# Kernel optimization log

Measured on AMD Instinct MI355X. Metric: run time of the kernel, lower is better.

Reference implementation:

```python
import jax, jax.numpy as jnp
import numpy as np
import math

K_HEADS = 16  # nb_heads from init_kwargs


def setup_inputs() -> dict:
    key = jax.random.key(0)
    ks = jax.random.split(key, 7)
    B, M, H, D = 2, 2048, 1024, 1024 // K_HEADS
    return {
        "h": jax.random.normal(ks[0], (B, M, H), jnp.float32),
        "h_cache": jax.random.normal(ks[1], (B, M, H), jnp.float32),
        "key_pe": jax.random.normal(ks[2], (1, D, M), jnp.float32),
        "Wq": jax.random.normal(ks[3], (H, H), jnp.float32) * 0.02,
        "Wk": jax.random.normal(ks[4], (H, H), jnp.float32) * 0.02,
        "Wv": jax.random.normal(ks[5], (H, H), jnp.float32) * 0.02,
        "Wo": jax.random.normal(ks[6], (H, H), jnp.float32) * 0.02,
    }


def _heads(x, K):
    # [B, M, H] -> [B, K, M, D]
    B, M, H = x.shape
    return x.reshape(B, M, K, H // K).transpose(0, 2, 1, 3)


def reference(h, h_cache, key_pe, Wq, Wk, Wv, Wo):
    B, M, H = h.shape
    K = K_HEADS
    D = H // K
    q = _heads(h @ Wq.T, K)        # [B, K, M, D]
    k = _heads(h_cache @ Wk.T, K)  # [B, K, L, D], L == M
    v = _heads(h_cache @ Wv.T, K)  # [B, K, L, D]

    attn_cont = jnp.einsum("bkmd,bkld->bkml", q, k)            # content scores
    attn_pos = jnp.einsum("bkmd,dl->bkml", q, key_pe[0])       # positional scores
    attn = (attn_cont + attn_pos[..., :M]) / math.sqrt(D)
    attn = jax.nn.softmax(attn, axis=-1)  # computed as in source, but source
    # (faithfully) multiplies VALUE by attn_cont, not attn:
    out = jnp.einsum("bkml,bkld->bkmd", attn_cont, v)          # [B, K, M, D]
    out = out.transpose(0, 2, 1, 3).reshape(B, M, H)
    return out @ Wo.T
```

## Files before the change

kernel.cpp:

```cpp
#include <hip/hip_runtime.h>
#include <hip/hip_bf16.h>

#define BB 2
#define MM 2048
#define HH 1024
#define KH 16

typedef short s16x8 __attribute__((ext_vector_type(8)));
typedef float f32x4 __attribute__((ext_vector_type(4)));
typedef float f32x16 __attribute__((ext_vector_type(16)));

#define GLOBAL_AS __attribute__((address_space(1)))
#define LDS_AS    __attribute__((address_space(3)))

__device__ __forceinline__ void async_copy16(const void* g, void* l) {
    __builtin_amdgcn_global_load_lds((const GLOBAL_AS void*)g, (LDS_AS void*)l, 16, 0, 0);
}

struct __align__(8) bf16x4_t { __hip_bfloat16 x, y, z, w; };

__global__ __launch_bounds__(256) void cvt_all(
    const float* __restrict__ s0, const float* __restrict__ s1,
    const float* __restrict__ s2, const float* __restrict__ s3,
    const float* __restrict__ s4, const float* __restrict__ Wq,
    __hip_bfloat16* __restrict__ d0, __hip_bfloat16* __restrict__ d1,
    __hip_bfloat16* __restrict__ d2, __hip_bfloat16* __restrict__ d3,
    __hip_bfloat16* __restrict__ d4, __hip_bfloat16* __restrict__ WqT,
    float* __restrict__ Sz)
{
    const int seg = blockIdx.y;
    const int t = threadIdx.x;
    if (seg == 5) {
        const int bx = blockIdx.x;
        if (bx < 128) {
            const int i = (bx * 256 + t) * 4;
            float4 z = {0.f, 0.f, 0.f, 0.f};
            *(float4*)(Sz + i) = z;
        } else if (bx < 384) {
            __shared__ float Tl[64][65];
            const int tile = bx - 128;
            const int j0 = (tile >> 4) * 64;
            const int k0 = (tile & 15) * 64;
            const int r = t >> 6;
            const int c = t & 63;
#pragma unroll
            for (int i = 0; i < 64; i += 4)
                Tl[r + i][c] = Wq[(size_t)(j0 + r + i) * HH + k0 + c];
            __syncthreads();
#pragma unroll
            for (int i = 0; i < 64; i += 4)
                WqT[(size_t)(k0 + r + i) * HH + j0 + c] = __float2bfloat16(Tl[c][r + i]);
        }
        return;
    }
    const float* src;
    __hip_bfloat16* dst;
    int n;
    switch (seg) {
        case 0: src = s0; dst = d0; n = BB * MM * HH; break;
        case 1: src = s1; dst = d1; n = BB * MM * HH; break;
        case 2: src = s2; dst = d2; n = HH * HH; break;
        case 3: src = s3; dst = d3; n = HH * HH; break;
        default: src = s4; dst = d4; n = HH * HH; break;
    }
    const int i = (blockIdx.x * 256 + t) * 4;
    if (i + 3 < n) {
        const float4 v = *(const float4*)(src + i);
        bf16x4_t o;
        o.x = __float2bfloat16(v.x);
        o.y = __float2bfloat16(v.y);
        o.z = __float2bfloat16(v.z);
        o.w = __float2bfloat16(v.w);
        *(bf16x4_t*)(dst + i) = o;
    }
}

__device__ __forceinline__ void store_c(__hip_bfloat16* C, size_t idx, float v) {
    C[idx] = __float2bfloat16(v);
}
__device__ __forceinline__ void store_c(float* C, size_t idx, float v) { C[idx] = v; }

#define LP2 136

__global__ __launch_bounds__(256) void gemm_kvt(
    const __hip_bfloat16* __restrict__ hcb,
    const __hip_bfloat16* __restrict__ wk, const __hip_bfloat16* __restrict__ wv,
    float* __restrict__ S)
{
    __shared__ __align__(16) char smem[64 * LP2 * 2 * 2];
    __hip_bfloat16* As  = (__hip_bfloat16*)smem;
    __hip_bfloat16* Bsk = (__hip_bfloat16*)(smem + 16384);
    __hip_bfloat16* Bsv = (__hip_bfloat16*)(smem + 24576);
    __hip_bfloat16* Kt  = (__hip_bfloat16*)smem;
    __hip_bfloat16* Vt  = (__hip_bfloat16*)(smem + 64 * LP2 * 2);

    const int t    = threadIdx.x;
    const int lane = t & 63;
    const int wave = t >> 6;
    const int head = blockIdx.y;
    const int m0   = blockIdx.x * 128;
    const int n0   = head * 64;
    const int b    = blockIdx.x >> 4;

    const int srow = lane >> 3;
    const int sw   = ((lane & 7) ^ srow) * 8;

    const int wm  = (wave >> 1) * 64;
    const int wn  = (wave & 1) * 32;
    const int fm  = lane & 31;
    const int fm7 = fm & 7;
    const int ghi = lane >> 5;

    f32x16 acck[2] = {};
    f32x16 accv[2] = {};

    for (int k0 = 0; k0 < HH; k0 += 64) {
        __syncthreads();
#pragma unroll
        for (int i = 0; i < 4; ++i) {
            const int c = wave * 4 + i;
            async_copy16(hcb + (size_t)(m0 + c * 8 + srow) * HH + k0 + sw,
                         As + c * 512);
        }
#pragma unroll
        for (int i = 0; i < 2; ++i) {
            const int c = wave * 2 + i;
            async_copy16(wk + (size_t)(n0 + c * 8 + srow) * HH + k0 + sw,
                         Bsk + c * 512);
            async_copy16(wv + (size_t)(n0 + c * 8 + srow) * HH + k0 + sw,
                         Bsv + c * 512);
        }
        __syncthreads();

#pragma unroll
        for (int ks = 0; ks < 64; ks += 16) {
            const int pos = ((((ks >> 3) + ghi) ^ fm7) * 8);
            s16x8 af[2];
#pragma unroll
            for (int mi = 0; mi < 2; ++mi)
                af[mi] = *(const s16x8*)(As + (wm + mi * 32 + fm) * 64 + pos);
            const s16x8 bk = *(const s16x8*)(Bsk + (wn + fm) * 64 + pos);
            const s16x8 bv = *(const s16x8*)(Bsv + (wn + fm) * 64 + pos);
#pragma unroll
            for (int mi = 0; mi < 2; ++mi) {
                acck[mi] = __builtin_amdgcn_mfma_f32_32x32x16_bf16(af[mi], bk, acck[mi], 0, 0, 0);
                accv[mi] = __builtin_amdgcn_mfma_f32_32x32x16_bf16(af[mi], bv, accv[mi], 0, 0, 0);
            }
        }
    }

    __syncthreads();

    const int dcol = wn + (lane & 31);
    const int lhi  = 4 * (lane >> 5);
#pragma unroll
    for (int mi = 0; mi < 2; ++mi)
#pragma unroll
        for (int g = 0; g < 4; ++g) {
            const int lb = wm + mi * 32 + 8 * g + lhi;
            bf16x4_t ok, ov;
            ok.x = __float2bfloat16(acck[mi][4 * g + 0]);
            ok.y = __float2bfloat16(acck[mi][4 * g + 1]);
            ok.z = __float2bfloat16(acck[mi][4 * g + 2]);
            ok.w = __float2bfloat16(acck[mi][4 * g + 3]);
            ov.x = __float2bfloat16(accv[mi][4 * g + 0]);
            ov.y = __float2bfloat16(accv[mi][4 * g + 1]);
            ov.z = __float2bfloat16(accv[mi][4 * g + 2]);
            ov.w = __float2bfloat16(accv[mi][4 * g + 3]);
            *(bf16x4_t*)(Kt + dcol * LP2 + lb) = ok;
            *(bf16x4_t*)(Vt + dcol * LP2 + lb) = ov;
        }
    __syncthreads();

    const int fr = lane & 15;
    const int fq = (lane >> 4) * 8;
    const int wm2 = wave * 16;

    f32x4 acc2[4] = {};
#pragma unroll
    for (int kk = 0; kk < 128; kk += 32) {
        const s16x8 af = *(const s16x8*)(Kt + (wm2 + fr) * LP2 + kk + fq);
        s16x8 bf[4];
#pragma unroll
        for (int nj = 0; nj < 4; ++nj)
            bf[nj] = *(const s16x8*)(Vt + (nj * 16 + fr) * LP2 + kk + fq);
#pragma unroll
        for (int nj = 0; nj < 4; ++nj)
            acc2[nj] = __builtin_amdgcn_mfma_f32_16x16x32_bf16(af, bf[nj], acc2[nj], 0, 0, 0);
    }

    float* Sg = S + ((size_t)b * KH + head) * 4096;
    const int er = (lane >> 4) * 4;
    const int ec = lane & 15;
#pragma unroll
    for (int nj = 0; nj < 4; ++nj)
#pragma unroll
        for (int rr = 0; rr < 4; ++rr)
            atomicAdd(&Sg[(wm2 + er + rr) * 64 + nj * 16 + ec], acc2[nj][rr]);
}

template <typename OutT>
__device__ __forceinline__ void gemm_nt_body64_m64(
    const __hip_bfloat16* __restrict__ A,
    const __hip_bfloat16* __restrict__ Bm,
    OutT* __restrict__ C,
    __hip_bfloat16* As, __hip_bfloat16* Bs,
    int m0, int n0)
{
    const int t    = threadIdx.x;
    const int lane = t & 63;
    const int wave = t >> 6;

    const int srow = lane >> 3;
    const int sw   = ((lane & 7) ^ srow) * 8;

    const int wn  = wave * 32;
    const int fm  = lane & 31;
    const int fm7 = fm & 7;
    const int ghi = lane >> 5;

    f32x16 acc[2] = {};

    for (int k0 = 0; k0 < HH; k0 += 64) {
        __syncthreads();
        {
            const __hip_bfloat16* ag = A + (size_t)(m0 + wave * 16 + srow) * HH + k0 + sw;
            async_copy16(ag,          As + wave * 1024);
            async_copy16(ag + 8 * HH, As + wave * 1024 + 512);
        }
#pragma unroll
        for (int i = 0; i < 2; ++i) {
            const int c = wave * 2 + i;
            const __hip_bfloat16* bg = Bm + (size_t)(n0 + c * 16 + srow) * HH + k0 + sw;
            async_copy16(bg,          Bs + c * 1024);
            async_copy16(bg + 8 * HH, Bs + c * 1024 + 512);
        }
        __syncthreads();

#pragma unroll
        for (int ks = 0; ks < 64; ks += 16) {
            const int pos = ((((ks >> 3) + ghi) ^ fm7) * 8);
            s16x8 af[2], bf;
#pragma unroll
            for (int mi = 0; mi < 2; ++mi)
                af[mi] = *(const s16x8*)(As + (mi * 32 + fm) * 64 + pos);
            bf = *(const s16x8*)(Bs + (wn + fm) * 64 + pos);
#pragma unroll
            for (int mi = 0; mi < 2; ++mi)
                acc[mi] = __builtin_amdgcn_mfma_f32_32x32x16_bf16(
                    af[mi], bf, acc[mi], 0, 0, 0);
        }
    }

    const int ec = lane & 31;
    const int eb = (lane >> 5) * 4;
#pragma unroll
    for (int mi = 0; mi < 2; ++mi)
#pragma unroll
        for (int r = 0; r < 16; ++r) {
            const int m = m0 + mi * 32 + (r & 3) + 8 * (r >> 2) + eb;
            const int n = n0 + wn + ec;
            store_c(C, (size_t)m * HH + n, acc[mi][r]);
        }
}

__global__ __launch_bounds__(256) void gemm_f(
    const __hip_bfloat16* __restrict__ W2, const __hip_bfloat16* __restrict__ WqT,
    __hip_bfloat16* __restrict__ F)
{
    __shared__ __align__(16) __hip_bfloat16 As[64 * 64];
    __shared__ __align__(16) __hip_bfloat16 Bs[128 * 64];
    const int b = blockIdx.z;
    gemm_nt_body64_m64(W2 + (size_t)b * HH * HH, WqT, F + (size_t)b * HH * HH,
                       As, Bs, blockIdx.x * 64, blockIdx.y * 128);
}

__global__ __launch_bounds__(256) void gemm_final(
    const __hip_bfloat16* __restrict__ hb, const __hip_bfloat16* __restrict__ F,
    float* __restrict__ outg)
{
    __shared__ __align__(16) __hip_bfloat16 As[64 * 64];
    __shared__ __align__(16) __hip_bfloat16 Bs[128 * 64];
    const int b = blockIdx.z;
    gemm_nt_body64_m64(hb + (size_t)b * MM * HH, F + (size_t)b * HH * HH,
                       outg + (size_t)b * MM * HH, As, Bs,
                       blockIdx.x * 64, blockIdx.y * 128);
}

__global__ __launch_bounds__(256) void w2_fold(
    const __hip_bfloat16* __restrict__ Wo,
    const float* __restrict__ S,
    __hip_bfloat16* __restrict__ W2)
{
    __shared__ float Sl[64 * 68];
    __shared__ float Wl[128 * 68];
    const int t = threadIdx.x, head = blockIdx.y, b = blockIdx.z;
    const int n0 = blockIdx.x * 128;

    const float* Sg = S + ((size_t)b * KH + head) * 4096;
    for (int idx = t; idx < 4096; idx += 256) {
        const int dp = idx >> 6, d = idx & 63;
        Sl[d * 68 + dp] = Sg[idx];
    }
    for (int idx = t; idx < 1024; idx += 256) {
        const int r = idx >> 3, c8 = (idx & 7) * 8;
        s16x8 wv = *(const s16x8*)(Wo + (size_t)(n0 + r) * HH + head * 64 + c8);
#pragma unroll
        for (int j = 0; j < 8; ++j) {
            __hip_bfloat16 wb = *(((const __hip_bfloat16*)&wv) + j);
            Wl[r * 68 + c8 + j] = __bfloat162float(wb);
        }
    }
    __syncthreads();

    const int dpb = (t & 15) * 4;
    const int ng  = t >> 4;
    float acc[8][4] = {};
    for (int d0 = 0; d0 < 64; d0 += 4) {
        f32x4 sv[4];
#pragma unroll
        for (int r = 0; r < 4; ++r)
            sv[r] = *(const f32x4*)(Sl + (d0 + r) * 68 + dpb);
#pragma unroll
        for (int i = 0; i < 8; ++i) {
            const f32x4 wv = *(const f32x4*)(Wl + (ng + 16 * i) * 68 + d0);
#pragma unroll
            for (int r = 0; r < 4; ++r)
#pragma unroll
                for (int j = 0; j < 4; ++j)
                    acc[i][j] += wv[r] * sv[r][j];
        }
    }

#pragma unroll
    for (int i = 0; i < 8; ++i) {
        bf16x4_t o;
        o.x = __float2bfloat16(acc[i][0]);
        o.y = __float2bfloat16(acc[i][1]);
        o.z = __float2bfloat16(acc[i][2]);
        o.w = __float2bfloat16(acc[i][3]);
        *(bf16x4_t*)(W2 + (size_t)b * HH * HH + (size_t)(n0 + ng + 16 * i) * HH
                     + head * 64 + dpb) = o;
    }
}

extern "C" void kernel_launch(void* const* d_in, const int* in_sizes, int n_in,
                              void* d_out, int out_size, void* d_ws, size_t ws_size,
                              hipStream_t stream) {
    const float* h_f  = (const float*)d_in[0];
    const float* hc_f = (const float*)d_in[1];
    const float* Wq_f = (const float*)d_in[3];
    const float* Wk_f = (const float*)d_in[4];
    const float* Wv_f = (const float*)d_in[5];
    const float* Wo_f = (const float*)d_in[6];
    float* out = (float*)d_out;

    const size_t act_b = (size_t)BB * MM * HH * 2;
    const size_t w_b   = (size_t)HH * HH * 2;
    char* ws = (char*)d_ws;
    __hip_bfloat16* hb   = (__hip_bfloat16*)(ws);
    __hip_bfloat16* hcb  = (__hip_bfloat16*)(ws + act_b);
    __hip_bfloat16* wkb  = (__hip_bfloat16*)(ws + 2 * act_b);
    __hip_bfloat16* wvb  = (__hip_bfloat16*)(ws + 2 * act_b + w_b);
    __hip_bfloat16* wob  = (__hip_bfloat16*)(ws + 2 * act_b + 2 * w_b);
    __hip_bfloat16* wqt  = (__hip_bfloat16*)(ws + 2 * act_b + 3 * w_b);
    float*          Sbuf = (float*)(ws + 2 * act_b + 4 * w_b);
    __hip_bfloat16* W2   = (__hip_bfloat16*)(ws + 2 * act_b + 4 * w_b + (size_t)512 * 1024);
    __hip_bfloat16* Fbuf = (__hip_bfloat16*)(ws + 2 * act_b + 6 * w_b + (size_t)512 * 1024);

    const dim3 blk(256);

    cvt_all<<<dim3(4096, 6), blk, 0, stream>>>(h_f, hc_f, Wk_f, Wv_f, Wo_f, Wq_f,
                                               hb, hcb, wkb, wvb, wob, wqt, Sbuf);

    gemm_kvt<<<dim3(32, KH), blk, 0, stream>>>(hcb, wkb, wvb, Sbuf);

    w2_fold<<<dim3(8, KH, BB), blk, 0, stream>>>(wob, Sbuf, W2);

    gemm_f<<<dim3(16, 8, 2), blk, 0, stream>>>(W2, wqt, Fbuf);

    gemm_final<<<dim3(32, 8, 2), blk, 0, stream>>>(hb, Fbuf, out);
}
```

Measured before the change: 164.7 us.

## Reassociate per-head K^T V via Gram matrix of h_cache instead of fused KV GEMM

Replaces the fused K/V projection plus per-head K^T V kernel (with atomics) with a reassociated chain. It transposes h_cache to bf16 during conversion, then computes the Gram matrix G = hc^T hc per batch, then V2 = Wv G, then per-head S = Wk_h V2_h^T. This removes the atomic accumulation and zero-init of S. In exchange it adds extra full 1024x1024 GEMMs, a transposed conversion pass and more workspace. Precision changes because G is rounded to bf16 before the later products.

```diff
diff --git a/kernel.cpp b/kernel.cpp
--- a/kernel.cpp
+++ b/kernel.cpp
@@ -20,50 +20,62 @@
 struct __align__(8) bf16x4_t { __hip_bfloat16 x, y, z, w; };
 
 __global__ __launch_bounds__(256) void cvt_all(
-    const float* __restrict__ s0, const float* __restrict__ s1,
-    const float* __restrict__ s2, const float* __restrict__ s3,
-    const float* __restrict__ s4, const float* __restrict__ Wq,
-    __hip_bfloat16* __restrict__ d0, __hip_bfloat16* __restrict__ d1,
-    __hip_bfloat16* __restrict__ d2, __hip_bfloat16* __restrict__ d3,
-    __hip_bfloat16* __restrict__ d4, __hip_bfloat16* __restrict__ WqT,
-    float* __restrict__ Sz)
-{
+    const float* __restrict__ h_f, const float* __restrict__ hc_f,
+    const float* __restrict__ Wk_f, const float* __restrict__ Wv_f,
+    const float* __restrict__ Wo_f, const float* __restrict__ Wq_f,
+    __hip_bfloat16* __restrict__ hb, __hip_bfloat16* __restrict__ hcT,
+    __hip_bfloat16* __restrict__ wkb, __hip_bfloat16* __restrict__ wvb,
+    __hip_bfloat16* __restrict__ wob, __hip_bfloat16* __restrict__ wqt)
+{
+    __shared__ float Tl[64][65];
     const int seg = blockIdx.y;
     const int t = threadIdx.x;
+    const int bx = blockIdx.x;
+
+    if (seg == 1) {
+        if (bx >= BB * 512) return;
+        const int b = bx >> 9;
+        const int tile = bx & 511;
+        const int m0 = (tile >> 4) * 64;
+        const int k0 = (tile & 15) * 64;
+        const int r = t >> 6;
+        const int c = t & 63;
+        const float* src = hc_f + (size_t)b * MM * HH;
+#pragma unroll
+        for (int i = 0; i < 64; i += 4)
+            Tl[r + i][c] = src[(size_t)(m0 + r + i) * HH + k0 + c];
+        __syncthreads();
+        __hip_bfloat16* dst = hcT + (size_t)b * HH * MM;
+#pragma unroll
+        for (int i = 0; i < 64; i += 4)
+            dst[(size_t)(k0 + r + i) * MM + m0 + c] = __float2bfloat16(Tl[c][r + i]);
+        return;
+    }
     if (seg == 5) {
-        const int bx = blockIdx.x;
-        if (bx < 128) {
-            const int i = (bx * 256 + t) * 4;
-            float4 z = {0.f, 0.f, 0.f, 0.f};
-            *(float4*)(Sz + i) = z;
-        } else if (bx < 384) {
-            __shared__ float Tl[64][65];
-            const int tile = bx - 128;
-            const int j0 = (tile >> 4) * 64;
-            const int k0 = (tile & 15) * 64;
-            const int r = t >> 6;
-            const int c = t & 63;
-#pragma unroll
-            for (int i = 0; i < 64; i += 4)
-                Tl[r + i][c] = Wq[(size_t)(j0 + r + i) * HH + k0 + c];
-            __syncthreads();
-#pragma unroll
-            for (int i = 0; i < 64; i += 4)
-                WqT[(size_t)(k0 + r + i) * HH + j0 + c] = __float2bfloat16(Tl[c][r + i]);
-        }
+        if (bx >= 256) return;
+        const int j0 = (bx >> 4) * 64;
+        const int k0 = (bx & 15) * 64;
+        const int r = t >> 6;
+        const int c = t & 63;
+#pragma unroll
+        for (int i = 0; i < 64; i += 4)
+            Tl[r + i][c] = Wq_f[(size_t)(j0 + r + i) * HH + k0 + c];
+        __syncthreads();
+#pragma unroll
+        for (int i = 0; i < 64; i += 4)
+            wqt[(size_t)(k0 + r + i) * HH + j0 + c] = __float2bfloat16(Tl[c][r + i]);
         return;
     }
     const float* src;
     __hip_bfloat16* dst;
     int n;
     switch (seg) {
-        case 0: src = s0; dst = d0; n = BB * MM * HH; break;
-        case 1: src = s1; dst = d1; n = BB * MM * HH; break;
-        case 2: src = s2; dst = d2; n = HH * HH; break;
-        case 3: src = s3; dst = d3; n = HH * HH; break;
-        default: src = s4; dst = d4; n = HH * HH; break;
-    }
-    const int i = (blockIdx.x * 256 + t) * 4;
+        case 0: src = h_f;  dst = hb;  n = BB * MM * HH; break;
+        case 2: src = Wk_f; dst = wkb; n = HH * HH; break;
+        case 3: src = Wv_f; dst = wvb; n = HH * HH; break;
+        default: src = Wo_f; dst = wob; n = HH * HH; break;
+    }
+    const int i = (bx * 256 + t) * 4;
     if (i + 3 < n) {
         const float4 v = *(const float4*)(src + i);
         bf16x4_t o;
@@ -80,132 +92,13 @@
 }
 __device__ __forceinline__ void store_c(float* C, size_t idx, float v) { C[idx] = v; }
 
-#define LP2 136
-
-__global__ __launch_bounds__(256) void gemm_kvt(
-    const __hip_bfloat16* __restrict__ hcb,
-    const __hip_bfloat16* __restrict__ wk, const __hip_bfloat16* __restrict__ wv,
-    float* __restrict__ S)
-{
-    __shared__ __align__(16) char smem[64 * LP2 * 2 * 2];
-    __hip_bfloat16* As  = (__hip_bfloat16*)smem;
-    __hip_bfloat16* Bsk = (__hip_bfloat16*)(smem + 16384);
-    __hip_bfloat16* Bsv = (__hip_bfloat16*)(smem + 24576);
-    __hip_bfloat16* Kt  = (__hip_bfloat16*)smem;
-    __hip_bfloat16* Vt  = (__hip_bfloat16*)(smem + 64 * LP2 * 2);
-
-    const int t    = threadIdx.x;
-    const int lane = t & 63;
-    const int wave = t >> 6;
-    const int head = blockIdx.y;
-    const int m0   = blockIdx.x * 128;
-    const int n0   = head * 64;
-    const int b    = blockIdx.x >> 4;
-
-    const int srow = lane >> 3;
-    const int sw   = ((lane & 7) ^ srow) * 8;
-
-    const int wm  = (wave >> 1) * 64;
-    const int wn  = (wave & 1) * 32;
-    const int fm  = lane & 31;
-    const int fm7 = fm & 7;
-    const int ghi = lane >> 5;
-
-    f32x16 acck[2] = {};
-    f32x16 accv[2] = {};
-
-    for (int k0 = 0; k0 < HH; k0 += 64) {
-        __syncthreads();
-#pragma unroll
-        for (int i = 0; i < 4; ++i) {
-            const int c = wave * 4 + i;
-            async_copy16(hcb + (size_t)(m0 + c * 8 + srow) * HH + k0 + sw,
-                         As + c * 512);
-        }
-#pragma unroll
-        for (int i = 0; i < 2; ++i) {
-            const int c = wave * 2 + i;
-            async_copy16(wk + (size_t)(n0 + c * 8 + srow) * HH + k0 + sw,
-                         Bsk + c * 512);
-            async_copy16(wv + (size_t)(n0 + c * 8 + srow) * HH + k0 + sw,
-                         Bsv + c * 512);
-        }
-        __syncthreads();
-
-#pragma unroll
-        for (int ks = 0; ks < 64; ks += 16) {
-            const int pos = ((((ks >> 3) + ghi) ^ fm7) * 8);
-            s16x8 af[2];
-#pragma unroll
-            for (int mi = 0; mi < 2; ++mi)
-                af[mi] = *(const s16x8*)(As + (wm + mi * 32 + fm) * 64 + pos);
-            const s16x8 bk = *(const s16x8*)(Bsk + (wn + fm) * 64 + pos);
-            const s16x8 bv = *(const s16x8*)(Bsv + (wn + fm) * 64 + pos);
-#pragma unroll
-            for (int mi = 0; mi < 2; ++mi) {
-                acck[mi] = __builtin_amdgcn_mfma_f32_32x32x16_bf16(af[mi], bk, acck[mi], 0, 0, 0);
-                accv[mi] = __builtin_amdgcn_mfma_f32_32x32x16_bf16(af[mi], bv, accv[mi], 0, 0, 0);
-            }
-        }
-    }
-
-    __syncthreads();
-
-    const int dcol = wn + (lane & 31);
-    const int lhi  = 4 * (lane >> 5);
-#pragma unroll
-    for (int mi = 0; mi < 2; ++mi)
-#pragma unroll
-        for (int g = 0; g < 4; ++g) {
-            const int lb = wm + mi * 32 + 8 * g + lhi;
-            bf16x4_t ok, ov;
-            ok.x = __float2bfloat16(acck[mi][4 * g + 0]);
-            ok.y = __float2bfloat16(acck[mi][4 * g + 1]);
-            ok.z = __float2bfloat16(acck[mi][4 * g + 2]);
-            ok.w = __float2bfloat16(acck[mi][4 * g + 3]);
-            ov.x = __float2bfloat16(accv[mi][4 * g + 0]);
-            ov.y = __float2bfloat16(accv[mi][4 * g + 1]);
-            ov.z = __float2bfloat16(accv[mi][4 * g + 2]);
-            ov.w = __float2bfloat16(accv[mi][4 * g + 3]);
-            *(bf16x4_t*)(Kt + dcol * LP2 + lb) = ok;
-            *(bf16x4_t*)(Vt + dcol * LP2 + lb) = ov;
-        }
-    __syncthreads();
-
-    const int fr = lane & 15;
-    const int fq = (lane >> 4) * 8;
-    const int wm2 = wave * 16;
-
-    f32x4 acc2[4] = {};
-#pragma unroll
-    for (int kk = 0; kk < 128; kk += 32) {
-        const s16x8 af = *(const s16x8*)(Kt + (wm2 + fr) * LP2 + kk + fq);
-        s16x8 bf[4];
-#pragma unroll
-        for (int nj = 0; nj < 4; ++nj)
-            bf[nj] = *(const s16x8*)(Vt + (nj * 16 + fr) * LP2 + kk + fq);
-#pragma unroll
-        for (int nj = 0; nj < 4; ++nj)
-            acc2[nj] = __builtin_amdgcn_mfma_f32_16x16x32_bf16(af, bf[nj], acc2[nj], 0, 0, 0);
-    }
-
-    float* Sg = S + ((size_t)b * KH + head) * 4096;
-    const int er = (lane >> 4) * 4;
-    const int ec = lane & 15;
-#pragma unroll
-    for (int nj = 0; nj < 4; ++nj)
-#pragma unroll
-        for (int rr = 0; rr < 4; ++rr)
-            atomicAdd(&Sg[(wm2 + er + rr) * 64 + nj * 16 + ec], acc2[nj][rr]);
-}
-
-template <typename OutT>
-__device__ __forceinline__ void gemm_nt_body64_m64(
+template <typename OutT, int KD>
+__device__ __forceinline__ void gemm_nt_body64(
     const __hip_bfloat16* __restrict__ A,
     const __hip_bfloat16* __restrict__ Bm,
     OutT* __restrict__ C,
     __hip_bfloat16* As, __hip_bfloat16* Bs,
-    int m0, int n0)
+    int m0, int n0, int ldc)
 {
     const int t    = threadIdx.x;
     const int lane = t & 63;
@@ -221,19 +114,19 @@
 
     f32x16 acc[2] = {};
 
-    for (int k0 = 0; k0 < HH; k0 += 64) {
+    for (int k0 = 0; k0 < KD; k0 += 64) {
         __syncthreads();
         {
-            const __hip_bfloat16* ag = A + (size_t)(m0 + wave * 16 + srow) * HH + k0 + sw;
+            const __hip_bfloat16* ag = A + (size_t)(m0 + wave * 16 + srow) * KD + k0 + sw;
             async_copy16(ag,          As + wave * 1024);
-            async_copy16(ag + 8 * HH, As + wave * 1024 + 512);
+            async_copy16(ag + 8 * KD, As + wave * 1024 + 512);
         }
 #pragma unroll
         for (int i = 0; i < 2; ++i) {
             const int c = wave * 2 + i;
-            const __hip_bfloat16* bg = Bm + (size_t)(n0 + c * 16 + srow) * HH + k0 + sw;
+            const __hip_bfloat16* bg = Bm + (size_t)(n0 + c * 16 + srow) * KD + k0 + sw;
             async_copy16(bg,          Bs + c * 1024);
-            async_copy16(bg + 8 * HH, Bs + c * 1024 + 512);
+            async_copy16(bg + 8 * KD, Bs + c * 1024 + 512);
         }
         __syncthreads();
 
@@ -260,8 +153,84 @@
         for (int r = 0; r < 16; ++r) {
             const int m = m0 + mi * 32 + (r & 3) + 8 * (r >> 2) + eb;
             const int n = n0 + wn + ec;
-            store_c(C, (size_t)m * HH + n, acc[mi][r]);
-        }
+            store_c(C, (size_t)m * ldc + n, acc[mi][r]);
+        }
+}
+
+__global__ __launch_bounds__(256) void gemm_g(
+    const __hip_bfloat16* __restrict__ hcT, __hip_bfloat16* __restrict__ G)
+{
+    __shared__ __align__(16) __hip_bfloat16 As[64 * 64];
+    __shared__ __align__(16) __hip_bfloat16 Bs[128 * 64];
+    const int b = blockIdx.z;
+    const __hip_bfloat16* Ab = hcT + (size_t)b * HH * MM;
+    gemm_nt_body64<__hip_bfloat16, MM>(Ab, Ab, G + (size_t)b * HH * HH,
+                                       As, Bs, blockIdx.x * 64, blockIdx.y * 128, HH);
+}
+
+__global__ __launch_bounds__(256) void gemm_v2(
+    const __hip_bfloat16* __restrict__ wvb, const __hip_bfloat16* __restrict__ G,
+    __hip_bfloat16* __restrict__ V2T)
+{
+    __shared__ __align__(16) __hip_bfloat16 As[64 * 64];
+    __shared__ __align__(16) __hip_bfloat16 Bs[128 * 64];
+    const int b = blockIdx.z;
+    gemm_nt_body64<__hip_bfloat16, HH>(wvb, G + (size_t)b * HH * HH,
+                                       V2T + (size_t)b * HH * HH,
+                                       As, Bs, blockIdx.x * 64, blockIdx.y * 128, HH);
+}
+
+__global__ __launch_bounds__(256) void gemm_t(
+    const __hip_bfloat16* __restrict__ wk,
+    const __hip_bfloat16* __restrict__ v2t,
+    float* __restrict__ S)
+{
+    __shared__ __align__(16) __hip_bfloat16 As[64 * 64];
+    __shared__ __align__(16) __hip_bfloat16 Bs[64 * 64];
+    const int t    = threadIdx.x;
+    const int lane = t & 63;
+    const int wave = t >> 6;
+    const int head = blockIdx.x;
+    const int b    = blockIdx.y;
+
+    const __hip_bfloat16* A  = wk  + (size_t)head * 64 * HH;
+    const __hip_bfloat16* Bm = v2t + (size_t)b * HH * HH + (size_t)head * 64 * HH;
+
+    const int srow = lane >> 3;
+    const int sw   = ((lane & 7) ^ srow) * 8;
+    const int wm   = (wave >> 1) * 32;
+    const int wn   = (wave & 1) * 32;
+    const int fm   = lane & 31;
+    const int fm7  = fm & 7;
+    const int ghi  = lane >> 5;
+
+    f32x16 acc = {};
+    for (int k0 = 0; k0 < HH; k0 += 64) {
+        __syncthreads();
+#pragma unroll
+        for (int i = 0; i < 2; ++i) {
+            const int c = wave * 2 + i;
+            async_copy16(A  + (size_t)(c * 8 + srow) * HH + k0 + sw, As + c * 512);
+            async_copy16(Bm + (size_t)(c * 8 + srow) * HH + k0 + sw, Bs + c * 512);
+        }
+        __syncthreads();
+#pragma unroll
+        for (int ks = 0; ks < 64; ks += 16) {
+            const int pos = ((((ks >> 3) + ghi) ^ fm7) * 8);
+            const s16x8 af = *(const s16x8*)(As + (wm + fm) * 64 + pos);
+            const s16x8 bf = *(const s16x8*)(Bs + (wn + fm) * 64 + pos);
+            acc = __builtin_amdgcn_mfma_f32_32x32x16_bf16(af, bf, acc, 0, 0, 0);
+        }
+    }
+
+    float* Sg = S + ((size_t)b * KH + head) * 4096;
+    const int col   = lane & 31;
+    const int rbase = 4 * (lane >> 5);
+#pragma unroll
+    for (int r = 0; r < 16; ++r) {
+        const int row = (r & 3) + 8 * (r >> 2) + rbase;
+        Sg[(wm + row) * 64 + wn + col] = acc[r];
+    }
 }
 
 __global__ __launch_bounds__(256) void gemm_f(
@@ -271,8 +240,9 @@
     __shared__ __align__(16) __hip_bfloat16 As[64 * 64];
     __shared__ __align__(16) __hip_bfloat16 Bs[128 * 64];
     const int b = blockIdx.z;
-    gemm_nt_body64_m64(W2 + (size_t)b * HH * HH, WqT, F + (size_t)b * HH * HH,
-                       As, Bs, blockIdx.x * 64, blockIdx.y * 128);
+    gemm_nt_body64<__hip_bfloat16, HH>(W2 + (size_t)b * HH * HH, WqT,
+                                       F + (size_t)b * HH * HH,
+                                       As, Bs, blockIdx.x * 64, blockIdx.y * 128, HH);
 }
 
 __global__ __launch_bounds__(256) void gemm_final(
@@ -282,9 +252,9 @@
     __shared__ __align__(16) __hip_bfloat16 As[64 * 64];
     __shared__ __align__(16) __hip_bfloat16 Bs[128 * 64];
     const int b = blockIdx.z;
-    gemm_nt_body64_m64(hb + (size_t)b * MM * HH, F + (size_t)b * HH * HH,
-                       outg + (size_t)b * MM * HH, As, Bs,
-                       blockIdx.x * 64, blockIdx.y * 128);
+    gemm_nt_body64<float, HH>(hb + (size_t)b * MM * HH, F + (size_t)b * HH * HH,
+                              outg + (size_t)b * MM * HH, As, Bs,
+                              blockIdx.x * 64, blockIdx.y * 128, HH);
 }
 
 __global__ __launch_bounds__(256) void w2_fold(
@@ -359,25 +329,31 @@
     const size_t w_b   = (size_t)HH * HH * 2;
     char* ws = (char*)d_ws;
     __hip_bfloat16* hb   = (__hip_bfloat16*)(ws);
-    __hip_bfloat16* hcb  = (__hip_bfloat16*)(ws + act_b);
+    __hip_bfloat16* hcT  = (__hip_bfloat16*)(ws + act_b);
     __hip_bfloat16* wkb  = (__hip_bfloat16*)(ws + 2 * act_b);
     __hip_bfloat16* wvb  = (__hip_bfloat16*)(ws + 2 * act_b + w_b);
     __hip_bfloat16* wob  = (__hip_bfloat16*)(ws + 2 * act_b + 2 * w_b);
     __hip_bfloat16* wqt  = (__hip_bfloat16*)(ws + 2 * act_b + 3 * w_b);
-    float*          Sbuf = (float*)(ws + 2 * act_b + 4 * w_b);
-    __hip_bfloat16* W2   = (__hip_bfloat16*)(ws + 2 * act_b + 4 * w_b + (size_t)512 * 1024);
-    __hip_bfloat16* Fbuf = (__hip_bfloat16*)(ws + 2 * act_b + 6 * w_b + (size_t)512 * 1024);
+    __hip_bfloat16* Gb   = (__hip_bfloat16*)(ws + 2 * act_b + 4 * w_b);
+    __hip_bfloat16* V2T  = (__hip_bfloat16*)(ws + 2 * act_b + 6 * w_b);
+    float*          Sbuf = (float*)(ws + 2 * act_b + 8 * w_b);
+    __hip_bfloat16* W2   = (__hip_bfloat16*)(ws + 2 * act_b + 8 * w_b + (size_t)512 * 1024);
+    __hip_bfloat16* Fbuf = (__hip_bfloat16*)(ws + 2 * act_b + 10 * w_b + (size_t)512 * 1024);
 
     const dim3 blk(256);
 
     cvt_all<<<dim3(4096, 6), blk, 0, stream>>>(h_f, hc_f, Wk_f, Wv_f, Wo_f, Wq_f,
-                                               hb, hcb, wkb, wvb, wob, wqt, Sbuf);
-
-    gemm_kvt<<<dim3(32, KH), blk, 0, stream>>>(hcb, wkb, wvb, Sbuf);
+                                               hb, hcT, wkb, wvb, wob, wqt);
+
+    gemm_g<<<dim3(16, 8, BB), blk, 0, stream>>>(hcT, Gb);
+
+    gemm_v2<<<dim3(16, 8, BB), blk, 0, stream>>>(wvb, Gb, V2T);
+
+    gemm_t<<<dim3(KH, BB), blk, 0, stream>>>(wkb, V2T, Sbuf);
 
     w2_fold<<<dim3(8, KH, BB), blk, 0, stream>>>(wob, Sbuf, W2);
 
-    gemm_f<<<dim3(16, 8, 2), blk, 0, stream>>>(W2, wqt, Fbuf);
-
-    gemm_final<<<dim3(32, 8, 2), blk, 0, stream>>>(hb, Fbuf, out);
-}
+    gemm_f<<<dim3(16, 8, BB), blk, 0, stream>>>(W2, wqt, Fbuf);
+
+    gemm_final<<<dim3(32, 8, BB), blk, 0, stream>>>(hb, Fbuf, out);
+}
```

Result: slower. 190.3 us (+15.5%).

## Compute Q projection directly, fused into the K/V launch, dropping the weight-fold GEMM

Applied to the files above, without the earlier changes.

The pipeline previously folded Wq into the per-batch weight product (gemm_f) and then multiplied the input h by that folded matrix. It now computes Q = h·Wqᵀ in extra blocks of the same launch as the K/V score-accumulation kernel, and the final GEMM multiplies Q by W2. The Wq transpose in the conversion kernel becomes a plain bf16 cast, and one launch and one intermediate buffer go away. The trade is more total GEMM FLOPs (a 4096-row projection instead of two 1024×1024 products), in exchange for better grid fill from running it concurrently with the K/V work.

```diff
diff --git a/kernel.cpp b/kernel.cpp
--- a/kernel.cpp
+++ b/kernel.cpp
@@ -25,7 +25,7 @@
     const float* __restrict__ s4, const float* __restrict__ Wq,
     __hip_bfloat16* __restrict__ d0, __hip_bfloat16* __restrict__ d1,
     __hip_bfloat16* __restrict__ d2, __hip_bfloat16* __restrict__ d3,
-    __hip_bfloat16* __restrict__ d4, __hip_bfloat16* __restrict__ WqT,
+    __hip_bfloat16* __restrict__ d4, __hip_bfloat16* __restrict__ wqb,
     float* __restrict__ Sz)
 {
     const int seg = blockIdx.y;
@@ -36,20 +36,15 @@
             const int i = (bx * 256 + t) * 4;
             float4 z = {0.f, 0.f, 0.f, 0.f};
             *(float4*)(Sz + i) = z;
-        } else if (bx < 384) {
-            __shared__ float Tl[64][65];
-            const int tile = bx - 128;
-            const int j0 = (tile >> 4) * 64;
-            const int k0 = (tile & 15) * 64;
-            const int r = t >> 6;
-            const int c = t & 63;
-#pragma unroll
-            for (int i = 0; i < 64; i += 4)
-                Tl[r + i][c] = Wq[(size_t)(j0 + r + i) * HH + k0 + c];
-            __syncthreads();
-#pragma unroll
-            for (int i = 0; i < 64; i += 4)
-                WqT[(size_t)(k0 + r + i) * HH + j0 + c] = __float2bfloat16(Tl[c][r + i]);
+        } else if (bx < 1152) {
+            const int i = ((bx - 128) * 256 + t) * 4;
+            const float4 v = *(const float4*)(Wq + i);
+            bf16x4_t o;
+            o.x = __float2bfloat16(v.x);
+            o.y = __float2bfloat16(v.y);
+            o.z = __float2bfloat16(v.z);
+            o.w = __float2bfloat16(v.w);
+            *(bf16x4_t*)(wqb + i) = o;
         }
         return;
     }
@@ -80,27 +75,107 @@
 }
 __device__ __forceinline__ void store_c(float* C, size_t idx, float v) { C[idx] = v; }
 
+template <typename OutT>
+__device__ __forceinline__ void gemm_nt_body64_m64(
+    const __hip_bfloat16* __restrict__ A,
+    const __hip_bfloat16* __restrict__ Bm,
+    OutT* __restrict__ C,
+    __hip_bfloat16* As, __hip_bfloat16* Bs,
+    int m0, int n0)
+{
+    const int t    = threadIdx.x;
+    const int lane = t & 63;
+    const int wave = t >> 6;
+
+    const int srow = lane >> 3;
+    const int sw   = ((lane & 7) ^ srow) * 8;
+
+    const int wn  = wave * 32;
+    const int fm  = lane & 31;
+    const int fm7 = fm & 7;
+    const int ghi = lane >> 5;
+
+    f32x16 acc[2] = {};
+
+    for (int k0 = 0; k0 < HH; k0 += 64) {
+        __syncthreads();
+        {
+            const __hip_bfloat16* ag = A + (size_t)(m0 + wave * 16 + srow) * HH + k0 + sw;
+            async_copy16(ag,          As + wave * 1024);
+            async_copy16(ag + 8 * HH, As + wave * 1024 + 512);
+        }
+#pragma unroll
+        for (int i = 0; i < 2; ++i) {
+            const int c = wave * 2 + i;
+            const __hip_bfloat16* bg = Bm + (size_t)(n0 + c * 16 + srow) * HH + k0 + sw;
+            async_copy16(bg,          Bs + c * 1024);
+            async_copy16(bg + 8 * HH, Bs + c * 1024 + 512);
+        }
+        __syncthreads();
+
+#pragma unroll
+        for (int ks = 0; ks < 64; ks += 16) {
+            const int pos = ((((ks >> 3) + ghi) ^ fm7) * 8);
+            s16x8 af[2], bf;
+#pragma unroll
+            for (int mi = 0; mi < 2; ++mi)
+                af[mi] = *(const s16x8*)(As + (mi * 32 + fm) * 64 + pos);
+            bf = *(const s16x8*)(Bs + (wn + fm) * 64 + pos);
+#pragma unroll
+            for (int mi = 0; mi < 2; ++mi)
+                acc[mi] = __builtin_amdgcn_mfma_f32_32x32x16_bf16(
+                    af[mi], bf, acc[mi], 0, 0, 0);
+        }
+    }
+
+    const int ec = lane & 31;
+    const int eb = (lane >> 5) * 4;
+#pragma unroll
+    for (int mi = 0; mi < 2; ++mi)
+#pragma unroll
+        for (int r = 0; r < 16; ++r) {
+            const int m = m0 + mi * 32 + (r & 3) + 8 * (r >> 2) + eb;
+            const int n = n0 + wn + ec;
+            store_c(C, (size_t)m * HH + n, acc[mi][r]);
+        }
+}
+
 #define LP2 136
 
-__global__ __launch_bounds__(256) void gemm_kvt(
+__global__ __launch_bounds__(256) void mega_kvtq(
     const __hip_bfloat16* __restrict__ hcb,
     const __hip_bfloat16* __restrict__ wk, const __hip_bfloat16* __restrict__ wv,
-    float* __restrict__ S)
+    const __hip_bfloat16* __restrict__ hb, const __hip_bfloat16* __restrict__ wqb,
+    float* __restrict__ S, __hip_bfloat16* __restrict__ qb)
 {
     __shared__ __align__(16) char smem[64 * LP2 * 2 * 2];
+
+    const int t    = threadIdx.x;
+    const int lane = t & 63;
+    const int wave = t >> 6;
+    const int bx   = blockIdx.x;
+
+    if (bx >= 512) {
+        __hip_bfloat16* As = (__hip_bfloat16*)smem;
+        __hip_bfloat16* Bs = (__hip_bfloat16*)(smem + 8192);
+        const int idx = bx - 512;
+        const int m0 = (idx >> 3) * 64;
+        const int n0 = (idx & 7) * 128;
+        gemm_nt_body64_m64(hb, wqb, qb, As, Bs, m0, n0);
+        return;
+    }
+
     __hip_bfloat16* As  = (__hip_bfloat16*)smem;
     __hip_bfloat16* Bsk = (__hip_bfloat16*)(smem + 16384);
     __hip_bfloat16* Bsv = (__hip_bfloat16*)(smem + 24576);
     __hip_bfloat16* Kt  = (__hip_bfloat16*)smem;
     __hip_bfloat16* Vt  = (__hip_bfloat16*)(smem + 64 * LP2 * 2);
 
-    const int t    = threadIdx.x;
-    const int lane = t & 63;
-    const int wave = t >> 6;
-    const int head = blockIdx.y;
-    const int m0   = blockIdx.x * 128;
+    const int kx   = bx & 31;
+    const int head = bx >> 5;
+    const int m0   = kx * 128;
     const int n0   = head * 64;
-    const int b    = blockIdx.x >> 4;
+    const int b    = kx >> 4;
 
     const int srow = lane >> 3;
     const int sw   = ((lane & 7) ^ srow) * 8;
@@ -199,90 +274,14 @@
             atomicAdd(&Sg[(wm2 + er + rr) * 64 + nj * 16 + ec], acc2[nj][rr]);
 }
 
-template <typename OutT>
-__device__ __forceinline__ void gemm_nt_body64_m64(
-    const __hip_bfloat16* __restrict__ A,
-    const __hip_bfloat16* __restrict__ Bm,
-    OutT* __restrict__ C,
-    __hip_bfloat16* As, __hip_bfloat16* Bs,
-    int m0, int n0)
-{
-    const int t    = threadIdx.x;
-    const int lane = t & 63;
-    const int wave = t >> 6;
-
-    const int srow = lane >> 3;
-    const int sw   = ((lane & 7) ^ srow) * 8;
-
-    const int wn  = wave * 32;
-    const int fm  = lane & 31;
-    const int fm7 = fm & 7;
-    const int ghi = lane >> 5;
-
-    f32x16 acc[2] = {};
-
-    for (int k0 = 0; k0 < HH; k0 += 64) {
-        __syncthreads();
-        {
-            const __hip_bfloat16* ag = A + (size_t)(m0 + wave * 16 + srow) * HH + k0 + sw;
-            async_copy16(ag,          As + wave * 1024);
-            async_copy16(ag + 8 * HH, As + wave * 1024 + 512);
-        }
-#pragma unroll
-        for (int i = 0; i < 2; ++i) {
-            const int c = wave * 2 + i;
-            const __hip_bfloat16* bg = Bm + (size_t)(n0 + c * 16 + srow) * HH + k0 + sw;
-            async_copy16(bg,          Bs + c * 1024);
-            async_copy16(bg + 8 * HH, Bs + c * 1024 + 512);
-        }
-        __syncthreads();
-
-#pragma unroll
-        for (int ks = 0; ks < 64; ks += 16) {
-            const int pos = ((((ks >> 3) + ghi) ^ fm7) * 8);
-            s16x8 af[2], bf;
-#pragma unroll
-            for (int mi = 0; mi < 2; ++mi)
-                af[mi] = *(const s16x8*)(As + (mi * 32 + fm) * 64 + pos);
-            bf = *(const s16x8*)(Bs + (wn + fm) * 64 + pos);
-#pragma unroll
-            for (int mi = 0; mi < 2; ++mi)
-                acc[mi] = __builtin_amdgcn_mfma_f32_32x32x16_bf16(
-                    af[mi], bf, acc[mi], 0, 0, 0);
-        }
-    }
-
-    const int ec = lane & 31;
-    const int eb = (lane >> 5) * 4;
-#pragma unroll
-    for (int mi = 0; mi < 2; ++mi)
-#pragma unroll
-        for (int r = 0; r < 16; ++r) {
-            const int m = m0 + mi * 32 + (r & 3) + 8 * (r >> 2) + eb;
-            const int n = n0 + wn + ec;
-            store_c(C, (size_t)m * HH + n, acc[mi][r]);
-        }
-}
-
-__global__ __launch_bounds__(256) void gemm_f(
-    const __hip_bfloat16* __restrict__ W2, const __hip_bfloat16* __restrict__ WqT,
-    __hip_bfloat16* __restrict__ F)
+__global__ __launch_bounds__(256) void gemm_final(
+    const __hip_bfloat16* __restrict__ qb, const __hip_bfloat16* __restrict__ W2,
+    float* __restrict__ outg)
 {
     __shared__ __align__(16) __hip_bfloat16 As[64 * 64];
     __shared__ __align__(16) __hip_bfloat16 Bs[128 * 64];
     const int b = blockIdx.z;
-    gemm_nt_body64_m64(W2 + (size_t)b * HH * HH, WqT, F + (size_t)b * HH * HH,
-                       As, Bs, blockIdx.x * 64, blockIdx.y * 128);
-}
-
-__global__ __launch_bounds__(256) void gemm_final(
-    const __hip_bfloat16* __restrict__ hb, const __hip_bfloat16* __restrict__ F,
-    float* __restrict__ outg)
-{
-    __shared__ __align__(16) __hip_bfloat16 As[64 * 64];
-    __shared__ __align__(16) __hip_bfloat16 Bs[128 * 64];
-    const int b = blockIdx.z;
-    gemm_nt_body64_m64(hb + (size_t)b * MM * HH, F + (size_t)b * HH * HH,
+    gemm_nt_body64_m64(qb + (size_t)b * MM * HH, W2 + (size_t)b * HH * HH,
                        outg + (size_t)b * MM * HH, As, Bs,
                        blockIdx.x * 64, blockIdx.y * 128);
 }
@@ -363,21 +362,19 @@
     __hip_bfloat16* wkb  = (__hip_bfloat16*)(ws + 2 * act_b);
     __hip_bfloat16* wvb  = (__hip_bfloat16*)(ws + 2 * act_b + w_b);
     __hip_bfloat16* wob  = (__hip_bfloat16*)(ws + 2 * act_b + 2 * w_b);
-    __hip_bfloat16* wqt  = (__hip_bfloat16*)(ws + 2 * act_b + 3 * w_b);
-    float*          Sbuf = (float*)(ws + 2 * act_b + 4 * w_b);
-    __hip_bfloat16* W2   = (__hip_bfloat16*)(ws + 2 * act_b + 4 * w_b + (size_t)512 * 1024);
-    __hip_bfloat16* Fbuf = (__hip_bfloat16*)(ws + 2 * act_b + 6 * w_b + (size_t)512 * 1024);
+    __hip_bfloat16* wqb  = (__hip_bfloat16*)(ws + 2 * act_b + 3 * w_b);
+    __hip_bfloat16* qb   = (__hip_bfloat16*)(ws + 2 * act_b + 4 * w_b);
+    float*          Sbuf = (float*)(ws + 3 * act_b + 4 * w_b);
+    __hip_bfloat16* W2   = (__hip_bfloat16*)(ws + 3 * act_b + 4 * w_b + (size_t)512 * 1024);
 
     const dim3 blk(256);
 
     cvt_all<<<dim3(4096, 6), blk, 0, stream>>>(h_f, hc_f, Wk_f, Wv_f, Wo_f, Wq_f,
-                                               hb, hcb, wkb, wvb, wob, wqt, Sbuf);
-
-    gemm_kvt<<<dim3(32, KH), blk, 0, stream>>>(hcb, wkb, wvb, Sbuf);
+                                               hb, hcb, wkb, wvb, wob, wqb, Sbuf);
+
+    mega_kvtq<<<dim3(1024), blk, 0, stream>>>(hcb, wkb, wvb, hb, wqb, Sbuf, qb);
 
     w2_fold<<<dim3(8, KH, BB), blk, 0, stream>>>(wob, Sbuf, W2);
 
-    gemm_f<<<dim3(16, 8, 2), blk, 0, stream>>>(W2, wqt, Fbuf);
-
-    gemm_final<<<dim3(32, 8, 2), blk, 0, stream>>>(hb, Fbuf, out);
-}
+    gemm_final<<<dim3(32, 8, BB), blk, 0, stream>>>(qb, W2, out);
+}
```

Measured after the change: 163.6 us. Within noise of the previous version (-0.7%).
